# Kernel optimization log

Measured on AMD Instinct MI355X. Metric: run time of the kernel, lower is better.

## Reference

```python
import jax, jax.numpy as jnp
import numpy as np

NUM_BATCHES = 2


def _bn(x, gamma, beta, eps=1e-5):
    # training-mode BatchNorm1d over active-voxel rows (biased variance, as torch)
    mu = x.mean(axis=0)
    var = x.var(axis=0)
    return (x - mu) * jax.lax.rsqrt(var + eps) * gamma + beta


def setup_inputs() -> dict:
    rng = np.random.default_rng(0)
    B, Z, Y, X = 2, 8, 512, 512
    Cin, Cout, R = 64, 128, 16
    Yo, Xo = Y // 2, X // 2
    N = 200_000
    lin = np.sort(rng.choice(B * Z * Y * X, size=N, replace=False))
    b = lin // (Z * Y * X); r = lin % (Z * Y * X)
    z = r // (Y * X); r = r % (Y * X)
    y = r // X; x = r % X
    bz = b * Z + z
    # spconv rulebook for kernel (1,3,3), stride (1,2,2), pad (0,1,1)
    in_lists, out_lists = [], []
    for ky in range(3):
        for kx in range(3):
            oy2 = y + 1 - ky; ox2 = x + 1 - kx
            ok = ((oy2 >= 0) & (oy2 % 2 == 0) & (oy2 // 2 < Yo)
                  & (ox2 >= 0) & (ox2 % 2 == 0) & (ox2 // 2 < Xo))
            idx = np.nonzero(ok)[0]
            out_lin = (bz[idx] * Yo + oy2[idx] // 2) * Xo + ox2[idx] // 2
            in_lists.append(idx); out_lists.append(out_lin)
    all_out = np.concatenate(out_lists)
    uniq, inv = np.unique(all_out, return_inverse=True)
    M = uniq.shape[0]
    P = max(len(a) for a in in_lists)
    conv_in = np.full((9, P), N, dtype=np.int32)   # pad -> zero feature row
    conv_out = np.full((9, P), M, dtype=np.int32)  # pad -> dropped garbage row
    off = 0
    for k in range(9):
        L = len(in_lists[k])
        conv_in[k, :L] = in_lists[k]
        conv_out[k, :L] = inv[off:off + L]
        off += L
    # skip: kernel 1, stride (1,2,2) -> inputs with even (y,x); its output coords
    # are always present in the main conv output set (center tap ky=kx=1)
    skip_in = np.nonzero((y % 2 == 0) & (x % 2 == 0))[0].astype(np.int32)
    skip_lin = (bz[skip_in] * Yo + y[skip_in] // 2) * Xo + x[skip_in] // 2
    skip_out = np.searchsorted(uniq, skip_lin).astype(np.int32)
    batch_of_out = (uniq // (Z * Yo * Xo)).astype(np.int32)

    key = jax.random.key(0)
    ks = jax.random.split(key, 5)
    return dict(
        features=jax.random.normal(ks[0], (N, Cin), jnp.float32),
        W_conv=jax.random.normal(ks[1], (9, Cin, Cout), jnp.float32) / np.sqrt(9 * Cin),
        W_skip=jax.random.normal(ks[2], (Cin, Cout), jnp.float32) / np.sqrt(Cin),
        bn_gamma=jnp.ones((Cout,), jnp.float32), bn_beta=jnp.zeros((Cout,), jnp.float32),
        skip_bn_gamma=jnp.ones((Cout,), jnp.float32), skip_bn_beta=jnp.zeros((Cout,), jnp.float32),
        fc1=jax.random.normal(ks[3], (Cout, Cout // R), jnp.float32) / np.sqrt(Cout),
        fc2=jax.random.normal(ks[4], (Cout // R, Cout), jnp.float32) / np.sqrt(Cout // R),
        conv_in_idx=jnp.asarray(conv_in), conv_out_idx=jnp.asarray(conv_out),
        skip_in_idx=jnp.asarray(skip_in), skip_out_idx=jnp.asarray(skip_out),
        batch_of_out=jnp.asarray(batch_of_out))


def reference(features, W_conv, W_skip, bn_gamma, bn_beta, skip_bn_gamma,
              skip_bn_beta, fc1, fc2, conv_in_idx, conv_out_idx,
              skip_in_idx, skip_out_idx, batch_of_out):
    N, Cin = features.shape
    K, _, Cout = W_conv.shape
    M = batch_of_out.shape[0]
    feats_pad = jnp.concatenate([features, jnp.zeros((1, Cin), features.dtype)], 0)
    # sparse stride-2 conv: per-offset gather -> GEMM -> scatter-add
    out = jnp.zeros((M + 1, Cout), features.dtype)
    for k in range(K):  # 9 fixed kernel taps
        contrib = feats_pad[conv_in_idx[k]] @ W_conv[k]  # [P, Cout]
        out = out.at[conv_out_idx[k]].add(contrib)
    out = _bn(out[:M], bn_gamma, bn_beta)
    # 1x1 stride-2 skip branch, BN over its own active rows, scatter to out coords
    skip_feats = _bn(features[skip_in_idx] @ W_skip, skip_bn_gamma, skip_bn_beta)
    identity = jnp.zeros((M, Cout), features.dtype).at[skip_out_idx].set(skip_feats)
    # SparseGDSCA: per-batch global-avg descriptor -> SE channel attention
    sums = jax.ops.segment_sum(out, batch_of_out, num_segments=NUM_BATCHES)
    cnts = jax.ops.segment_sum(jnp.ones((M,), out.dtype), batch_of_out, num_segments=NUM_BATCHES)
    desc = sums / cnts[:, None]                              # [B, Cout]
    attn = jax.nn.sigmoid(jax.nn.relu(desc @ fc1) @ fc2)     # [B, Cout]
    out = out * attn[batch_of_out]
    return jax.nn.relu(out + identity)                        # [M, Cout]
```

## Files before the change

### kernel.cpp

```cpp
#include <hip/hip_runtime.h>

#define CIN 64
#define COUT 128
#define NC 64
#define NSB 32
#define LDT 132
#define SKB 256
#define SB 256

typedef __bf16 bf16x8 __attribute__((ext_vector_type(8)));
typedef __bf16 bf16x4 __attribute__((ext_vector_type(4)));
typedef float  f32x4  __attribute__((ext_vector_type(4)));

__global__ __launch_bounds__(256) void prep_kernel(
    const float* __restrict__ feats, __bf16* __restrict__ fb,
    const float* __restrict__ Wc, const float* __restrict__ Ws, __bf16* __restrict__ wf,
    const int* __restrict__ cin_idx, const int* __restrict__ cout_idx, int* __restrict__ tap_in,
    int* __restrict__ pat_arr,
    const int* __restrict__ sout, int* __restrict__ inv,
    const int* __restrict__ boo, int* __restrict__ msplit,
    int total8, int P, int cpb, int Ls, int N, int M,
    int nbA, int nbAB, int nbABC, int nbABCD)
{
    const int bid = blockIdx.x, t = threadIdx.x;
    if (bid < nbA) {
        const int i = bid * 256 + t;
        if (i >= total8) return;
        const int i8 = i * 8;
        const float4 x0 = *(const float4*)(feats + i8);
        const float4 x1 = *(const float4*)(feats + i8 + 4);
        bf16x8 v;
        v[0] = (__bf16)x0.x; v[1] = (__bf16)x0.y; v[2] = (__bf16)x0.z; v[3] = (__bf16)x0.w;
        v[4] = (__bf16)x1.x; v[5] = (__bf16)x1.y; v[6] = (__bf16)x1.z; v[7] = (__bf16)x1.w;
        *(bf16x8*)(fb + i8) = v;
    } else if (bid < nbAB) {
        const int id = (bid - nbA) * 256 + t;
        if (id >= 160 * 64) return;
        const int f = id >> 6, lane = id & 63;
        const float* W; int r;
        if (f < 144) { W = Wc + (size_t)(f >> 4) * CIN * COUT; r = f & 15; }
        else         { W = Ws;                                  r = f - 144; }
        const int c = r >> 1, s = r & 1;
        const int kbase = s * 32 + (lane >> 4) * 8;
        const int col = c * 16 + (lane & 15);
        bf16x8 v;
#pragma unroll
        for (int j = 0; j < 8; ++j) v[j] = (__bf16)W[(size_t)(kbase + j) * COUT + col];
        *(bf16x8*)(wf + ((size_t)f * 64 + lane) * 8) = v;
    } else if (bid < nbABC) {
        const int c = bid - nbAB;
        const int k = c / cpb;
        const int e = (c - k * cpb) * 256 + t;
        if (e >= P) return;
        const int oo = cout_idx[(size_t)k * P + e];
        if (oo < M) {
            tap_in[(size_t)k * M + oo] = cin_idx[(size_t)k * P + e];
            atomicOr(&pat_arr[oo], 1 << k);
        }
    } else if (bid < nbABCD) {
        const int i = (bid - nbABC) * 256 + t;
        if (i < Ls) inv[sout[i]] = i + 1;
    } else {
        if (t < 64) fb[(size_t)N * CIN + t] = (__bf16)0.f;
        if (t == 0) {
            int lo = 0, hi = M;
            while (lo < hi) { const int mid = (lo + hi) >> 1; if (boo[mid] < 1) lo = mid + 1; else hi = mid; }
            msplit[0] = lo;
        }
    }
}

__global__ __launch_bounds__(256) void pat_kernel(
    const int* __restrict__ pat_arr, int* __restrict__ bh, int M, int rpb)
{
    __shared__ int lh[512];
    const int t = threadIdx.x, bid = blockIdx.x;
    lh[t] = 0; lh[t + 256] = 0;
    __syncthreads();
    const int mend = min((bid + 1) * rpb, M);
    for (int m = bid * rpb + t; m < mend; m += 256)
        atomicAdd(&lh[pat_arr[m]], 1);
    __syncthreads();
    bh[bid * 512 + t]       = lh[t];
    bh[bid * 512 + t + 256] = lh[t + 256];
}

__global__ __launch_bounds__(512) void scan_kernel(
    int* __restrict__ bh, int* __restrict__ gtab,
    int* __restrict__ ng_dev, int N, int maxS)
{
    __shared__ int buf[512];
    const int p = threadIdx.x;
    int total = 0;
    for (int b = 0; b < SB; ++b) total += bh[b * 512 + p];
    const int pc = (total + 15) & ~15;
    buf[p] = pc;
    __syncthreads();
    for (int off = 1; off < 512; off <<= 1) {
        const int v = (p >= off) ? buf[p - off] : 0;
        __syncthreads();
        buf[p] += v;
        __syncthreads();
    }
    int running = buf[p] - pc;
    if (p == 511) ng_dev[0] = buf[511] >> 4;
    for (int b = 0; b < SB; ++b) {
        const int c = bh[b * 512 + p];
        bh[b * 512 + p] = running;
        running += c;
    }
    const int nslots = __builtin_popcount(p);
    for (int x = running; x < buf[p]; ++x)
        for (int s = 0; s < nslots; ++s) gtab[(size_t)s * maxS + x] = N;
}

__global__ __launch_bounds__(256) void scatter_kernel(
    const int* __restrict__ pat_arr, const int* __restrict__ bh,
    const int* __restrict__ tap_in,
    int* __restrict__ pos_arr, int* __restrict__ spat, int* __restrict__ boob,
    int* __restrict__ gtab,
    const int* __restrict__ boo, int M, int rpb, int maxS)
{
    __shared__ int lcur[512];
    const int t = threadIdx.x, bid = blockIdx.x;
    lcur[t]       = bh[bid * 512 + t];
    lcur[t + 256] = bh[bid * 512 + t + 256];
    __syncthreads();
    const int mend = min((bid + 1) * rpb, M);
    for (int m = bid * rpb + t; m < mend; m += 256) {
        const int p = pat_arr[m];
        const int pos = atomicAdd(&lcur[p], 1);
        pos_arr[m] = pos;
        spat[pos] = p;
        boob[pos] = boo[m];
        int slot = 0;
        for (int pk = p; pk; pk &= (pk - 1)) {
            const int k = __builtin_ctz(pk);
            gtab[(size_t)slot * maxS + pos] = tap_in[(size_t)k * M + m];
            ++slot;
        }
    }
}

__global__ __launch_bounds__(256, 4) void conv_mfma_kernel(
    const __bf16* __restrict__ fb,
    const __bf16* __restrict__ wf,
    const int* __restrict__ gtab,
    const int* __restrict__ spat,
    const int* __restrict__ boob,
    const int* __restrict__ ng_dev,
    const int* __restrict__ sin_idx,
    __bf16* __restrict__ raw,
    __bf16* __restrict__ G,
    float* __restrict__ zstats,
    int N, int M, int Ls, int maxS)
{
    __shared__ float tile[4 * 16 * LDT];
    __shared__ float wred[3][4][128];
    const int t = threadIdx.x, lane = t & 63, wv = t >> 6;
    const int arow = lane & 15, apart = lane >> 4;

    if (blockIdx.x < SKB) {
        const __bf16* wk = wf + ((size_t)144 * 64 + lane) * 8;
        const bf16x8 b00 = *(const bf16x8*)(wk + (size_t)(wv * 4 + 0) * 512);
        const bf16x8 b01 = *(const bf16x8*)(wk + (size_t)(wv * 4 + 1) * 512);
        const bf16x8 b10 = *(const bf16x8*)(wk + (size_t)(wv * 4 + 2) * 512);
        const bf16x8 b11 = *(const bf16x8*)(wk + (size_t)(wv * 4 + 3) * 512);
        const int colA = wv * 32 + arow;
        const int colB = colA + 16;

        float s1A = 0.f, s2A = 0.f, s1B = 0.f, s2B = 0.f;
        const int ngroups = (Ls + 15) >> 4;
        for (int g = blockIdx.x; g < ngroups; g += SKB) {
            const int e0 = g * 16;
            const int ea = e0 + arow;
            const int ii = (ea < Ls) ? sin_idx[ea] : 0;
            const __bf16* fr = fb + (size_t)ii * CIN + apart * 8;
            const bf16x8 a0 = *(const bf16x8*)fr;
            const bf16x8 a1 = *(const bf16x8*)(fr + 32);

            f32x4 dA = {0.f,0.f,0.f,0.f};
            f32x4 dB = {0.f,0.f,0.f,0.f};
            dA = __builtin_amdgcn_mfma_f32_16x16x32_bf16(a0, b00, dA, 0, 0, 0);
            dA = __builtin_amdgcn_mfma_f32_16x16x32_bf16(a1, b01, dA, 0, 0, 0);
            dB = __builtin_amdgcn_mfma_f32_16x16x32_bf16(a0, b10, dB, 0, 0, 0);
            dB = __builtin_amdgcn_mfma_f32_16x16x32_bf16(a1, b11, dB, 0, 0, 0);

            const int er = e0 + apart * 4;
#pragma unroll
            for (int j = 0; j < 4; ++j) {
                if (er + j < Ls) {
                    const float vA = dA[j], vB = dB[j];
                    G[(size_t)(er + j) * COUT + colA] = (__bf16)vA;
                    G[(size_t)(er + j) * COUT + colB] = (__bf16)vB;
                    s1A += vA; s2A += vA * vA;
                    s1B += vB; s2B += vB * vB;
                }
            }
        }
        s1A += __shfl_xor(s1A, 16); s1A += __shfl_xor(s1A, 32);
        s2A += __shfl_xor(s2A, 16); s2A += __shfl_xor(s2A, 32);
        s1B += __shfl_xor(s1B, 16); s1B += __shfl_xor(s1B, 32);
        s2B += __shfl_xor(s2B, 16); s2B += __shfl_xor(s2B, 32);
        if (apart == 0) {
            wred[0][0][colA] = s1A; wred[0][0][colB] = s1B;
            wred[1][0][colA] = s2A; wred[1][0][colB] = s2B;
        }
        __syncthreads();
        float* bucket = zstats + NC * 384 + (size_t)(blockIdx.x & (NSB - 1)) * 256;
        if (t < 128) {
            atomicAdd(&bucket[t],       wred[0][0][t]);
            atomicAdd(&bucket[128 + t], wred[1][0][t]);
        }
        return;
    }

    const int ng = ng_dev[0];
    const int g = (blockIdx.x - SKB) * 4 + wv;
    const bool live = g < ng;
    const int m0 = g * 16;

    f32x4 D[8];
#pragma unroll
    for (int c = 0; c < 8; ++c) D[c] = (f32x4){0.f,0.f,0.f,0.f};

    const int pattern = live ? spat[m0] : 0;

    int slot = 0;
    for (int pk = pattern; pk; pk &= (pk - 1)) {
        const int k = __builtin_ctz(pk);
        const int vi = gtab[(size_t)slot * maxS + m0 + arow];
        ++slot;
        const __bf16* f0 = fb + (size_t)vi * CIN + apart * 8;
        const bf16x8 a0 = *(const bf16x8*)f0;
        const bf16x8 a1 = *(const bf16x8*)(f0 + 32);
        const __bf16* wb = wf + ((size_t)(k * 16) * 64 + lane) * 8;
#pragma unroll
        for (int c = 0; c < 8; ++c) {
            const bf16x8 b0 = *(const bf16x8*)(wb + (size_t)(c * 2 + 0) * 512);
            const bf16x8 b1 = *(const bf16x8*)(wb + (size_t)(c * 2 + 1) * 512);
            D[c] = __builtin_amdgcn_mfma_f32_16x16x32_bf16(a0, b0, D[c], 0, 0, 0);
            D[c] = __builtin_amdgcn_mfma_f32_16x16x32_bf16(a1, b1, D[c], 0, 0, 0);
        }
    }

    float ssum[8], sq[8], s0[8];
#pragma unroll
    for (int c = 0; c < 8; ++c) { ssum[c] = 0.f; sq[c] = 0.f; s0[c] = 0.f; }
    int4 bb = {1, 1, 1, 1};
    if (live) bb = *(const int4*)&boob[m0 + apart * 4];
#pragma unroll
    for (int c = 0; c < 8; ++c) {
        const float v0 = D[c][0], v1 = D[c][1], v2 = D[c][2], v3 = D[c][3];
        ssum[c] += v0 + v1 + v2 + v3;
        sq[c]   += v0*v0 + v1*v1 + v2*v2 + v3*v3;
        if (bb.x == 0) s0[c] += v0;
        if (bb.y == 0) s0[c] += v1;
        if (bb.z == 0) s0[c] += v2;
        if (bb.w == 0) s0[c] += v3;
    }

    float* T = tile + wv * (16 * LDT);
#pragma unroll
    for (int c = 0; c < 8; ++c)
#pragma unroll
        for (int j = 0; j < 4; ++j)
            T[(apart * 4 + j) * LDT + c * 16 + arow] = D[c][j];
    if (live) {
#pragma unroll
        for (int i = 0; i < 8; ++i) {
            const int r = i * 2 + (lane >> 5);
            const int c4 = (lane & 31) * 4;
            const f32x4 vv = *(const f32x4*)&T[r * LDT + c4];
            bf16x4 o;
            o[0] = (__bf16)vv[0]; o[1] = (__bf16)vv[1];
            o[2] = (__bf16)vv[2]; o[3] = (__bf16)vv[3];
            *(bf16x4*)&raw[(size_t)(m0 + r) * 128 + c4] = o;
        }
    }

#pragma unroll
    for (int c = 0; c < 8; ++c) {
        ssum[c] += __shfl_xor(ssum[c], 16); ssum[c] += __shfl_xor(ssum[c], 32);
        s0[c]   += __shfl_xor(s0[c], 16);   s0[c]   += __shfl_xor(s0[c], 32);
        sq[c]   += __shfl_xor(sq[c], 16);   sq[c]   += __shfl_xor(sq[c], 32);
    }
    if (apart == 0) {
#pragma unroll
        for (int c = 0; c < 8; ++c) {
            const int col = c * 16 + arow;
            wred[0][wv][col] = s0[c];
            wred[1][wv][col] = ssum[c] - s0[c];
            wred[2][wv][col] = sq[c];
        }
    }
    __syncthreads();
    float* bucket = zstats + (size_t)(blockIdx.x & (NC - 1)) * 384;
    if (t < 128) {
        atomicAdd(&bucket[t],       wred[0][0][t] + wred[0][1][t] + wred[0][2][t] + wred[0][3][t]);
        atomicAdd(&bucket[128 + t], wred[1][0][t] + wred[1][1][t] + wred[1][2][t] + wred[1][3][t]);
        atomicAdd(&bucket[256 + t], wred[2][0][t] + wred[2][1][t] + wred[2][2][t] + wred[2][3][t]);
    }
}

__global__ __launch_bounds__(128) void params_kernel(
    const float* __restrict__ zstats,
    const int* __restrict__ msplit_p,
    const float* __restrict__ gamma, const float* __restrict__ beta,
    const float* __restrict__ sgamma, const float* __restrict__ sbeta,
    const float* __restrict__ fc1, const float* __restrict__ fc2,
    float* __restrict__ scale, float* __restrict__ shift,
    float* __restrict__ sscale, float* __restrict__ sshift,
    float* __restrict__ attn,
    int Ls, int M)
{
    __shared__ float desc[2][COUT];
    __shared__ float hid[2][8];
    const int ch = threadIdx.x;

    float s0 = 0.f, s1 = 0.f, q = 0.f;
    for (int b = 0; b < NC; ++b) {
        const float* st = zstats + (size_t)b * 384;
        s0 += st[ch]; s1 += st[128 + ch]; q += st[256 + ch];
    }
    float ss = 0.f, sqk = 0.f;
    const float* sk = zstats + NC * 384;
    for (int b = 0; b < NSB; ++b) {
        ss  += sk[(size_t)b * 256 + ch];
        sqk += sk[(size_t)b * 256 + 128 + ch];
    }

    const float c0 = (float)msplit_p[0], c1 = (float)M - c0;
    const float Mf = (float)M;
    const float mu  = (s0 + s1) / Mf;
    const float var = q / Mf - mu * mu;
    const float rs  = rsqrtf(var + 1e-5f);
    const float sc  = rs * gamma[ch];
    const float sh  = beta[ch] - mu * sc;
    scale[ch] = sc;
    shift[ch] = sh;
    desc[0][ch] = (s0 / c0) * sc + sh;
    desc[1][ch] = (s1 / c1) * sc + sh;

    const float lsf  = (float)Ls;
    const float mus  = ss / lsf;
    const float vars = sqk / lsf - mus * mus;
    const float rss  = rsqrtf(vars + 1e-5f);
    const float ssc  = rss * sgamma[ch];
    sscale[ch] = ssc;
    sshift[ch] = sbeta[ch] - mus * ssc;

    __syncthreads();
    if (ch < 16) {
        const int b = ch >> 3, h = ch & 7;
        float a = 0.f;
        for (int c = 0; c < COUT; ++c) a += desc[b][c] * fc1[c * 8 + h];
        hid[b][h] = fmaxf(a, 0.f);
    }
    __syncthreads();
    for (int b = 0; b < 2; ++b) {
        float a = 0.f;
        for (int h = 0; h < 8; ++h) a += hid[b][h] * fc2[h * COUT + ch];
        attn[b * COUT + ch] = 1.f / (1.f + expf(-a));
    }
}

__global__ __launch_bounds__(256) void final_kernel(
    const __bf16* __restrict__ raw,
    const int* __restrict__ pos_arr,
    const int* __restrict__ boo,
    float* __restrict__ out,
    const __bf16* __restrict__ G,
    const int* __restrict__ inv_skip,
    const float* __restrict__ scale, const float* __restrict__ shift,
    const float* __restrict__ sscale, const float* __restrict__ sshift,
    const float* __restrict__ attn,
    int M)
{
    const int t  = threadIdx.x;
    const int c4 = (t & 31) * 4;
    const int rw = t >> 5;
    const float4 sc  = *(const float4*)&scale[c4];
    const float4 sh  = *(const float4*)&shift[c4];
    const float4 ssc = *(const float4*)&sscale[c4];
    const float4 ssh = *(const float4*)&sshift[c4];
    const float4 at0 = *(const float4*)&attn[c4];
    const float4 at1 = *(const float4*)&attn[COUT + c4];

    for (int m = blockIdx.x * 8 + rw; m < M; m += gridDim.x * 8) {
        const int pos = pos_arr[m];
        const bf16x4 rv = *(const bf16x4*)&raw[(size_t)pos * COUT + c4];
        const int b = boo[m];
        const int j = inv_skip[m];
        const float4 av = b ? at1 : at0;
        float4 y;
        y.x = ((float)rv[0] * sc.x + sh.x) * av.x;
        y.y = ((float)rv[1] * sc.y + sh.y) * av.y;
        y.z = ((float)rv[2] * sc.z + sh.z) * av.z;
        y.w = ((float)rv[3] * sc.w + sh.w) * av.w;
        if (j > 0) {
            const bf16x4 gg = *(const bf16x4*)&G[(size_t)(j - 1) * COUT + c4];
            y.x += (float)gg[0] * ssc.x + ssh.x;
            y.y += (float)gg[1] * ssc.y + ssh.y;
            y.z += (float)gg[2] * ssc.z + ssh.z;
            y.w += (float)gg[3] * ssc.w + ssh.w;
        }
        y.x = y.x > 0.f ? y.x : 0.f;
        y.y = y.y > 0.f ? y.y : 0.f;
        y.z = y.z > 0.f ? y.z : 0.f;
        y.w = y.w > 0.f ? y.w : 0.f;
        *(float4*)&out[(size_t)m * COUT + c4] = y;
    }
}

extern "C" void kernel_launch(void* const* d_in, const int* in_sizes, int n_in,
                              void* d_out, int out_size, void* d_ws, size_t ws_size,
                              hipStream_t stream)
{
    const float* feats  = (const float*)d_in[0];
    const float* Wc     = (const float*)d_in[1];
    const float* Wsk    = (const float*)d_in[2];
    const float* gamma  = (const float*)d_in[3];
    const float* beta   = (const float*)d_in[4];
    const float* sgamma = (const float*)d_in[5];
    const float* sbeta  = (const float*)d_in[6];
    const float* fc1    = (const float*)d_in[7];
    const float* fc2    = (const float*)d_in[8];
    const int* cin_idx  = (const int*)d_in[9];
    const int* cout_idx = (const int*)d_in[10];
    const int* sin_idx  = (const int*)d_in[11];
    const int* sout_idx = (const int*)d_in[12];
    const int* boo      = (const int*)d_in[13];

    const int N  = in_sizes[0] / CIN;
    const int P  = in_sizes[9] / 9;
    const int Ls = in_sizes[11];
    const int M  = in_sizes[13];
    const int maxS = ((M + 15) & ~15) + 512 * 16;
    const int maxG = maxS >> 4;
    const int rpb = (M + SB - 1) / SB;

    float* out = (float*)d_out;

    char* ws = (char*)d_ws;
    __bf16* fb = (__bf16*)ws;
    size_t off = (size_t)(N + 1) * CIN * sizeof(__bf16);
    off = (off + 255) & ~(size_t)255;
    __bf16* wfrag = (__bf16*)(ws + off);
    off += (size_t)160 * 64 * 8 * sizeof(__bf16);
    off = (off + 255) & ~(size_t)255;
    int* tap_in = (int*)(ws + off);
    off += (size_t)9 * M * sizeof(int);
    off = (off + 255) & ~(size_t)255;
    __bf16* G = (__bf16*)(ws + off);
    off += (size_t)Ls * COUT * sizeof(__bf16);
    off = (off + 255) & ~(size_t)255;
    int* pos_arr = (int*)(ws + off);
    off += (size_t)M * sizeof(int);
    int* spat = (int*)(ws + off);
    off += (size_t)maxS * sizeof(int);
    int* boob = (int*)(ws + off);
    off += (size_t)maxS * sizeof(int);
    off = (off + 255) & ~(size_t)255;
    int* gtab = (int*)(ws + off);
    off += (size_t)9 * maxS * sizeof(int);
    off = (off + 255) & ~(size_t)255;
    __bf16* raw = (__bf16*)(ws + off);
    off += (size_t)maxS * COUT * sizeof(__bf16);
    off = (off + 255) & ~(size_t)255;
    int* bh = (int*)(ws + off);
    off += (size_t)SB * 512 * sizeof(int);
    int* ng_dev = (int*)(ws + off);
    off += 256;
    int* msplit = (int*)(ws + off);
    off += 256;
    float* params = (float*)(ws + off);
    float* scale = params, *shift = params + 128;
    float* sscale = params + 256, *sshift = params + 384, *attn = params + 512;
    off += 768 * sizeof(float);
    off = (off + 255) & ~(size_t)255;
    float* zstats = (float*)(ws + off);
    size_t zoff = off + (size_t)(NC * 384 + NSB * 256) * sizeof(float);
    int* pat_arr = (int*)(ws + zoff);
    zoff += (size_t)M * sizeof(int);
    int* inv_skip = (int*)(ws + zoff);
    zoff += (size_t)M * sizeof(int);

    hipMemsetAsync(zstats, 0, zoff - off, stream);

    const int total8 = N * CIN / 8;
    const int nbA = (total8 + 255) / 256;
    const int nbB = (160 * 64 + 255) / 256;
    const int cpb = (P + 255) / 256;
    const int nbAB = nbA + nbB;
    const int nbABC = nbAB + 9 * cpb;
    const int nbABCD = nbABC + (Ls + 255) / 256;
    prep_kernel<<<nbABCD + 1, 256, 0, stream>>>(
        feats, fb, Wc, Wsk, wfrag, cin_idx, cout_idx, tap_in, pat_arr,
        sout_idx, inv_skip, boo, msplit,
        total8, P, cpb, Ls, N, M, nbA, nbAB, nbABC, nbABCD);

    pat_kernel<<<SB, 256, 0, stream>>>(pat_arr, bh, M, rpb);
    scan_kernel<<<1, 512, 0, stream>>>(bh, gtab, ng_dev, N, maxS);
    scatter_kernel<<<SB, 256, 0, stream>>>(pat_arr, bh, tap_in, pos_arr, spat, boob,
                                           gtab, boo, M, rpb, maxS);

    conv_mfma_kernel<<<SKB + (maxG + 3) / 4, 256, 0, stream>>>(
        fb, wfrag, gtab, spat, boob, ng_dev, sin_idx,
        raw, G, zstats, N, M, Ls, maxS);

    params_kernel<<<1, 128, 0, stream>>>(
        zstats, msplit, gamma, beta, sgamma, sbeta, fc1, fc2,
        scale, shift, sscale, sshift, attn, Ls, M);

    final_kernel<<<2048, 256, 0, stream>>>(
        raw, pos_arr, boo, out, G, inv_skip,
        scale, shift, sscale, sshift, attn, M);
}
```

Baseline: 214.0 us.

## Parallelize pattern histogram scan and overlap feature bf16 conversion with scatter

The single-block serial scan over per-block pattern histograms is split in two. The histogram is now stored transposed, one block computes per-pattern totals and bin bases with vectorized reads, and a 512-block kernel does the per-pattern exclusive scan over source blocks and the parallel padding fill of gtab. The fp32-to-bf16 feature conversion moves out of the prep kernel and into the scatter kernel as extra blocks, so it runs alongside the scatter. This adds one kernel launch and extra workspace for the transposed histogram, in exchange for removing a long serial single-thread loop.

```diff
diff --git a/kernel.cpp b/kernel.cpp
--- a/kernel.cpp
+++ b/kernel.cpp
@@ -13,28 +13,18 @@
 typedef float  f32x4  __attribute__((ext_vector_type(4)));
 
 __global__ __launch_bounds__(256) void prep_kernel(
-    const float* __restrict__ feats, __bf16* __restrict__ fb,
+    __bf16* __restrict__ fb,
     const float* __restrict__ Wc, const float* __restrict__ Ws, __bf16* __restrict__ wf,
     const int* __restrict__ cin_idx, const int* __restrict__ cout_idx, int* __restrict__ tap_in,
     int* __restrict__ pat_arr,
     const int* __restrict__ sout, int* __restrict__ inv,
     const int* __restrict__ boo, int* __restrict__ msplit,
-    int total8, int P, int cpb, int Ls, int N, int M,
-    int nbA, int nbAB, int nbABC, int nbABCD)
+    int P, int cpb, int Ls, int N, int M,
+    int nbB, int nbBC, int nbBCD)
 {
     const int bid = blockIdx.x, t = threadIdx.x;
-    if (bid < nbA) {
-        const int i = bid * 256 + t;
-        if (i >= total8) return;
-        const int i8 = i * 8;
-        const float4 x0 = *(const float4*)(feats + i8);
-        const float4 x1 = *(const float4*)(feats + i8 + 4);
-        bf16x8 v;
-        v[0] = (__bf16)x0.x; v[1] = (__bf16)x0.y; v[2] = (__bf16)x0.z; v[3] = (__bf16)x0.w;
-        v[4] = (__bf16)x1.x; v[5] = (__bf16)x1.y; v[6] = (__bf16)x1.z; v[7] = (__bf16)x1.w;
-        *(bf16x8*)(fb + i8) = v;
-    } else if (bid < nbAB) {
-        const int id = (bid - nbA) * 256 + t;
+    if (bid < nbB) {
+        const int id = bid * 256 + t;
         if (id >= 160 * 64) return;
         const int f = id >> 6, lane = id & 63;
         const float* W; int r;
@@ -47,8 +37,8 @@
 #pragma unroll
         for (int j = 0; j < 8; ++j) v[j] = (__bf16)W[(size_t)(kbase + j) * COUT + col];
         *(bf16x8*)(wf + ((size_t)f * 64 + lane) * 8) = v;
-    } else if (bid < nbABC) {
-        const int c = bid - nbAB;
+    } else if (bid < nbBC) {
+        const int c = bid - nbB;
         const int k = c / cpb;
         const int e = (c - k * cpb) * 256 + t;
         if (e >= P) return;
@@ -57,8 +47,8 @@
             tap_in[(size_t)k * M + oo] = cin_idx[(size_t)k * P + e];
             atomicOr(&pat_arr[oo], 1 << k);
         }
-    } else if (bid < nbABCD) {
-        const int i = (bid - nbABC) * 256 + t;
+    } else if (bid < nbBCD) {
+        const int i = (bid - nbBC) * 256 + t;
         if (i < Ls) inv[sout[i]] = i + 1;
     } else {
         if (t < 64) fb[(size_t)N * CIN + t] = (__bf16)0.f;
@@ -71,7 +61,7 @@
 }
 
 __global__ __launch_bounds__(256) void pat_kernel(
-    const int* __restrict__ pat_arr, int* __restrict__ bh, int M, int rpb)
+    const int* __restrict__ pat_arr, int* __restrict__ bht, int M, int rpb)
 {
     __shared__ int lh[512];
     const int t = threadIdx.x, bid = blockIdx.x;
@@ -81,19 +71,25 @@
     for (int m = bid * rpb + t; m < mend; m += 256)
         atomicAdd(&lh[pat_arr[m]], 1);
     __syncthreads();
-    bh[bid * 512 + t]       = lh[t];
-    bh[bid * 512 + t + 256] = lh[t + 256];
-}
-
-__global__ __launch_bounds__(512) void scan_kernel(
-    int* __restrict__ bh, int* __restrict__ gtab,
-    int* __restrict__ ng_dev, int N, int maxS)
+    bht[(size_t)t * SB + bid]         = lh[t];
+    bht[(size_t)(t + 256) * SB + bid] = lh[t + 256];
+}
+
+__global__ __launch_bounds__(512) void scanT_kernel(
+    const int* __restrict__ bht, int* __restrict__ binbase, int* __restrict__ totg,
+    int* __restrict__ ng_dev)
 {
     __shared__ int buf[512];
     const int p = threadIdx.x;
-    int total = 0;
-    for (int b = 0; b < SB; ++b) total += bh[b * 512 + p];
-    const int pc = (total + 15) & ~15;
+    const int4* row = (const int4*)(bht + (size_t)p * SB);
+    int tot = 0;
+#pragma unroll
+    for (int i = 0; i < SB / 4; ++i) {
+        const int4 v = row[i];
+        tot += v.x + v.y + v.z + v.w;
+    }
+    totg[p] = tot;
+    const int pc = (tot + 15) & ~15;
     buf[p] = pc;
     __syncthreads();
     for (int off = 1; off < 512; off <<= 1) {
@@ -102,29 +98,65 @@
         buf[p] += v;
         __syncthreads();
     }
-    int running = buf[p] - pc;
+    binbase[p] = buf[p] - pc;
     if (p == 511) ng_dev[0] = buf[511] >> 4;
-    for (int b = 0; b < SB; ++b) {
-        const int c = bh[b * 512 + p];
-        bh[b * 512 + p] = running;
-        running += c;
-    }
+}
+
+__global__ __launch_bounds__(256) void scanB_kernel(
+    const int* __restrict__ bht, const int* __restrict__ binbase,
+    const int* __restrict__ totg,
+    int* __restrict__ bh, int* __restrict__ gtab, int N, int maxS)
+{
+    __shared__ int sbuf[256];
+    const int p = blockIdx.x, t = threadIdx.x;
+    const int v = bht[(size_t)p * SB + t];
+    sbuf[t] = v;
+    __syncthreads();
+    for (int off = 1; off < 256; off <<= 1) {
+        const int x = (t >= off) ? sbuf[t - off] : 0;
+        __syncthreads();
+        sbuf[t] += x;
+        __syncthreads();
+    }
+    const int base = binbase[p];
+    bh[(size_t)t * 512 + p] = base + sbuf[t] - v;
+
+    const int tot = totg[p];
+    const int padded = (tot + 15) & ~15;
+    const int cnt = padded - tot;
     const int nslots = __builtin_popcount(p);
-    for (int x = running; x < buf[p]; ++x)
-        for (int s = 0; s < nslots; ++s) gtab[(size_t)s * maxS + x] = N;
-}
-
-__global__ __launch_bounds__(256) void scatter_kernel(
+    for (int idx = t; idx < cnt * nslots; idx += 256) {
+        const int x = base + tot + idx / nslots;
+        const int s = idx - (idx / nslots) * nslots;
+        gtab[(size_t)s * maxS + x] = N;
+    }
+}
+
+__global__ __launch_bounds__(256) void scatfeat_kernel(
     const int* __restrict__ pat_arr, const int* __restrict__ bh,
     const int* __restrict__ tap_in,
     int* __restrict__ pos_arr, int* __restrict__ spat, int* __restrict__ boob,
     int* __restrict__ gtab,
-    const int* __restrict__ boo, int M, int rpb, int maxS)
-{
+    const int* __restrict__ boo,
+    const float* __restrict__ feats, __bf16* __restrict__ fb,
+    int M, int rpb, int maxS, int total8)
+{
+    const int t = threadIdx.x, bid = blockIdx.x;
+    if (bid >= SB) {
+        const int i = (bid - SB) * 256 + t;
+        if (i >= total8) return;
+        const int i8 = i * 8;
+        const float4 x0 = *(const float4*)(feats + i8);
+        const float4 x1 = *(const float4*)(feats + i8 + 4);
+        bf16x8 v;
+        v[0] = (__bf16)x0.x; v[1] = (__bf16)x0.y; v[2] = (__bf16)x0.z; v[3] = (__bf16)x0.w;
+        v[4] = (__bf16)x1.x; v[5] = (__bf16)x1.y; v[6] = (__bf16)x1.z; v[7] = (__bf16)x1.w;
+        *(bf16x8*)(fb + i8) = v;
+        return;
+    }
     __shared__ int lcur[512];
-    const int t = threadIdx.x, bid = blockIdx.x;
-    lcur[t]       = bh[bid * 512 + t];
-    lcur[t + 256] = bh[bid * 512 + t + 256];
+    lcur[t]       = bh[(size_t)bid * 512 + t];
+    lcur[t + 256] = bh[(size_t)bid * 512 + t + 256];
     __syncthreads();
     const int mend = min((bid + 1) * rpb, M);
     for (int m = bid * rpb + t; m < mend; m += 256) {
@@ -470,6 +502,12 @@
     off = (off + 255) & ~(size_t)255;
     int* bh = (int*)(ws + off);
     off += (size_t)SB * 512 * sizeof(int);
+    int* bht = (int*)(ws + off);
+    off += (size_t)512 * SB * sizeof(int);
+    int* binbase = (int*)(ws + off);
+    off += 512 * sizeof(int);
+    int* totg = (int*)(ws + off);
+    off += 512 * sizeof(int);
     int* ng_dev = (int*)(ws + off);
     off += 256;
     int* msplit = (int*)(ws + off);
@@ -489,21 +527,21 @@
     hipMemsetAsync(zstats, 0, zoff - off, stream);
 
     const int total8 = N * CIN / 8;
-    const int nbA = (total8 + 255) / 256;
     const int nbB = (160 * 64 + 255) / 256;
     const int cpb = (P + 255) / 256;
-    const int nbAB = nbA + nbB;
-    const int nbABC = nbAB + 9 * cpb;
-    const int nbABCD = nbABC + (Ls + 255) / 256;
-    prep_kernel<<<nbABCD + 1, 256, 0, stream>>>(
-        feats, fb, Wc, Wsk, wfrag, cin_idx, cout_idx, tap_in, pat_arr,
+    const int nbBC = nbB + 9 * cpb;
+    const int nbBCD = nbBC + (Ls + 255) / 256;
+    prep_kernel<<<nbBCD + 1, 256, 0, stream>>>(
+        fb, Wc, Wsk, wfrag, cin_idx, cout_idx, tap_in, pat_arr,
         sout_idx, inv_skip, boo, msplit,
-        total8, P, cpb, Ls, N, M, nbA, nbAB, nbABC, nbABCD);
-
-    pat_kernel<<<SB, 256, 0, stream>>>(pat_arr, bh, M, rpb);
-    scan_kernel<<<1, 512, 0, stream>>>(bh, gtab, ng_dev, N, maxS);
-    scatter_kernel<<<SB, 256, 0, stream>>>(pat_arr, bh, tap_in, pos_arr, spat, boob,
-                                           gtab, boo, M, rpb, maxS);
+        P, cpb, Ls, N, M, nbB, nbBC, nbBCD);
+
+    pat_kernel<<<SB, 256, 0, stream>>>(pat_arr, bht, M, rpb);
+    scanT_kernel<<<1, 512, 0, stream>>>(bht, binbase, totg, ng_dev);
+    scanB_kernel<<<512, 256, 0, stream>>>(bht, binbase, totg, bh, gtab, N, maxS);
+    scatfeat_kernel<<<SB + (total8 + 255) / 256, 256, 0, stream>>>(
+        pat_arr, bh, tap_in, pos_arr, spat, boob, gtab, boo,
+        feats, fb, M, rpb, maxS, total8);
 
     conv_mfma_kernel<<<SKB + (maxG + 3) / 4, 256, 0, stream>>>(
         fb, wfrag, gtab, spat, boob, ng_dev, sin_idx,
```

New measurement: 215.3 us. About the same (+0.6%).
